# Kernel optimization log

Hardware: AMD Instinct MI355X
Metric: run time of the kernel (lower is better)

The kernel has to match this reference:

```python
import jax, jax.numpy as jnp
import numpy as np

B, S, W = 64, 128, 16
VOCAB, CVOCAB = 50000, 100
WDIM, CDIM, NF = 300, 50, 50
KS = [3, 4, 5]
HID, NLAYERS, NLAB = 256, 2, 5
COMB = WDIM + NF * len(KS)  # 450


def glorot(key, shape):
    fan_in, fan_out = shape[-2], shape[-1]
    lim = jnp.sqrt(6.0 / (fan_in + fan_out))
    return jax.random.uniform(key, shape, minval=-lim, maxval=lim, dtype=jnp.float32)


def setup_inputs() -> dict:
    key = jax.random.key(0)
    ks = jax.random.split(key, 32)
    word_ids = jax.random.randint(ks[0], (B, S), 1, VOCAB)
    char_ids = jax.random.randint(ks[1], (B, S, W), 1, CVOCAB)
    labels = jax.random.randint(ks[2], (B, S), 0, NLAB)
    lengths = jax.random.randint(ks[3], (B,), S // 2, S + 1)
    # embeddings
    word_emb = jax.random.normal(ks[4], (VOCAB, WDIM), jnp.float32) * 0.1
    word_emb = word_emb.at[0].set(0.0)
    char_emb = jax.random.normal(ks[5], (CVOCAB, CDIM), jnp.float32) * 0.1
    char_emb = char_emb.at[0].set(0.0)
    # char conv kernels: [ks, CDIM, NF] each, plus bias
    conv_w = [glorot(ks[6 + i], (k, CDIM, NF)) for i, k in enumerate(KS)]
    conv_b = [jnp.zeros((NF,), jnp.float32) for _ in KS]
    # LSTM params per layer per direction: W_ih [in,4H], W_hh [H,4H], b [4H]
    lstm = []
    kidx = 10
    in_dim = COMB
    for layer in range(NLAYERS):
        for d in range(2):
            Wih = glorot(ks[kidx], (in_dim, 4 * HID)); kidx += 1
            Whh = glorot(ks[kidx], (HID, 4 * HID)); kidx += 1
            b = jnp.zeros((4 * HID,), jnp.float32)
            lstm.extend([Wih, Whh, b])
        in_dim = 2 * HID
    out_w = glorot(ks[kidx], (2 * HID, NLAB)); kidx += 1
    out_b = jnp.zeros((NLAB,), jnp.float32)
    crf_start = jax.random.normal(ks[kidx], (NLAB,), jnp.float32) * 0.1; kidx += 1
    crf_end = jax.random.normal(ks[kidx], (NLAB,), jnp.float32) * 0.1; kidx += 1
    crf_trans = jax.random.normal(ks[kidx], (NLAB, NLAB), jnp.float32) * 0.1
    d = {
        'word_ids': word_ids, 'char_ids': char_ids, 'labels': labels, 'lengths': lengths,
        'word_emb': word_emb, 'char_emb': char_emb,
        'conv_w3': conv_w[0], 'conv_b3': conv_b[0],
        'conv_w4': conv_w[1], 'conv_b4': conv_b[1],
        'conv_w5': conv_w[2], 'conv_b5': conv_b[2],
        'out_w': out_w, 'out_b': out_b,
        'crf_start': crf_start, 'crf_end': crf_end, 'crf_trans': crf_trans,
    }
    names = ['Wih', 'Whh', 'b']
    i = 0
    for layer in range(NLAYERS):
        for dname in ['f', 'r']:
            for n in names:
                d[f'lstm_{n}_l{layer}{dname}'] = lstm[i]; i += 1
    return d


def _conv1d_same(x, w, b, pad):
    # x: [N, L, Cin], w: [k, Cin, Cout] -> [N, L_out, Cout]
    out = jax.lax.conv_general_dilated(x, w, window_strides=(1,), padding=[(pad, pad)],
                                       dimension_numbers=('NWC', 'WIO', 'NWC'))
    return out + b


def _lstm_dir(x, Wih, Whh, b, reverse):
    # x: [B, S, in] -> [B, S, H]; gate order i,f,g,o (torch convention)
    xg = jnp.einsum('bsi,ij->bsj', x, Wih) + b  # [B,S,4H]
    if reverse:
        xg = xg[:, ::-1]
    def step(carry, g):
        h, c = carry
        g = g + h @ Whh
        i, f, gg, o = jnp.split(g, 4, axis=-1)
        i, f, o = jax.nn.sigmoid(i), jax.nn.sigmoid(f), jax.nn.sigmoid(o)
        c = f * c + i * jnp.tanh(gg)
        h = o * jnp.tanh(c)
        return (h, c), h
    h0 = jnp.zeros((x.shape[0], HID), x.dtype)
    _, hs = jax.lax.scan(step, (h0, h0), jnp.swapaxes(xg, 0, 1))
    hs = jnp.swapaxes(hs, 0, 1)
    if reverse:
        hs = hs[:, ::-1]
    return hs


def reference(word_ids, char_ids, labels, lengths, word_emb, char_emb,
              conv_w3, conv_b3, conv_w4, conv_b4, conv_w5, conv_b5,
              out_w, out_b, crf_start, crf_end, crf_trans,
              lstm_Wih_l0f, lstm_Whh_l0f, lstm_b_l0f,
              lstm_Wih_l0r, lstm_Whh_l0r, lstm_b_l0r,
              lstm_Wih_l1f, lstm_Whh_l1f, lstm_b_l1f,
              lstm_Wih_l1r, lstm_Whh_l1r, lstm_b_l1r):
    # char CNN
    ce = char_emb[char_ids.reshape(-1, W)]  # [B*S, W, CDIM]
    pooled = []
    for w, b, k in [(conv_w3, conv_b3, 3), (conv_w4, conv_b4, 4), (conv_w5, conv_b5, 5)]:
        o = jax.nn.relu(_conv1d_same(ce, w, b, k // 2))
        pooled.append(jnp.max(o, axis=1))  # [B*S, NF]
    char_repr = jnp.concatenate(pooled, axis=-1).reshape(B, S, NF * len(KS))
    we = word_emb[word_ids]
    x = jnp.concatenate([we, char_repr], axis=-1)  # [B,S,COMB]
    # BiLSTM 2 layers (dropout disabled / eval mode)
    h_f = _lstm_dir(x, lstm_Wih_l0f, lstm_Whh_l0f, lstm_b_l0f, False)
    h_r = _lstm_dir(x, lstm_Wih_l0r, lstm_Whh_l0r, lstm_b_l0r, True)
    x = jnp.concatenate([h_f, h_r], axis=-1)
    h_f = _lstm_dir(x, lstm_Wih_l1f, lstm_Whh_l1f, lstm_b_l1f, False)
    h_r = _lstm_dir(x, lstm_Wih_l1r, lstm_Whh_l1r, lstm_b_l1r, True)
    x = jnp.concatenate([h_f, h_r], axis=-1)
    emissions = jnp.einsum('bsh,hl->bsl', x, out_w) + out_b  # [B,S,NLAB]
    # CRF NLL (pytorch-crf, batch_first, reduction='mean')
    mask = (jnp.arange(S)[None, :] < lengths[:, None])  # [B,S] bool
    maskf = mask.astype(emissions.dtype)
    tags = labels  # already in [0,NLAB)
    # numerator: score of gold path
    em_score = jnp.take_along_axis(emissions, tags[..., None], axis=-1)[..., 0]  # [B,S]
    num = crf_start[tags[:, 0]] + em_score[:, 0]
    trans_score = crf_trans[tags[:, :-1], tags[:, 1:]]  # [B,S-1]
    num = num + jnp.sum((trans_score + em_score[:, 1:]) * maskf[:, 1:], axis=1)
    last_idx = lengths - 1
    last_tag = jnp.take_along_axis(tags, last_idx[:, None], axis=1)[:, 0]
    num = num + crf_end[last_tag]
    # denominator: forward algorithm via scan
    alpha0 = crf_start + emissions[:, 0]  # [B,NLAB]
    def step(alpha, inp):
        em_t, m_t = inp  # [B,NLAB], [B]
        nxt = jax.nn.logsumexp(alpha[:, :, None] + crf_trans[None], axis=1) + em_t
        alpha = jnp.where(m_t[:, None], nxt, alpha)
        return alpha, None
    alpha, _ = jax.lax.scan(step, alpha0,
                            (jnp.swapaxes(emissions[:, 1:], 0, 1), jnp.swapaxes(mask[:, 1:], 0, 1)))
    denom = jax.nn.logsumexp(alpha + crf_end[None], axis=1)  # [B]
    llh = num - denom
    return -jnp.mean(llh)
```

## Files before the change

### kernel.cpp

```cpp
#include <hip/hip_runtime.h>
#include <hip/hip_fp16.h>
#include <math.h>
#include <stdint.h>

#define NB   64
#define NS   128
#define NW   16
#define CD   50
#define NF_  50
#define WD   300
#define COMB 450
#define K2P0 240
#define K2P1 256
#define HID  256
#define G4   1024
#define NLAB 5

#define WHH_SW4  (7.0f / 0.06846532f)
#define WHH_INV4 (1.0f / (WHH_SW4 * 7.0f))

#define CW_S   (7.0f / 0.24494897f)
#define EMB_S  14.0f
#define CONV_INV (1.0f / (CW_S * EMB_S))

typedef _Float16 h2_t __attribute__((ext_vector_type(2)));
typedef _Float16 v8h  __attribute__((ext_vector_type(8)));
typedef float    v16f __attribute__((ext_vector_type(16)));

__device__ __forceinline__ float sigf(float x)   { return 1.0f / (1.0f + __expf(-x)); }
__device__ __forceinline__ float tanhf_(float x) { return 1.0f - 2.0f / (__expf(2.0f * x) + 1.0f); }

__device__ __forceinline__ int sdot8f(uint32_t a, int b, int acc) {
#if __has_builtin(__builtin_amdgcn_sdot8)
    return __builtin_amdgcn_sdot8((int)a, b, acc, false);
#else
#pragma unroll
    for (int i = 0; i < 8; ++i) {
        int av = ((int)(a << (28 - 4 * i))) >> 28;
        int bv = ((int)(((uint32_t)b) << (28 - 4 * i))) >> 28;
        acc += av * bv;
    }
    return acc;
#endif
}

__device__ __forceinline__ uint32_t packh2(float lo, float hi) {
    __half l = __float2half(lo), h = __float2half(hi);
    return ((uint32_t)__half_as_ushort(h) << 16) | (uint32_t)__half_as_ushort(l);
}

__device__ __forceinline__ int q4clamp(float v, float s) {
    int q = (int)rintf(v * s);
    return q < -7 ? -7 : (q > 7 ? 7 : q);
}

#define PK_CONV_END 17
#define PK_WIH0_END (17 + 1920)
#define PK_WIH1_END (PK_WIH0_END + 2048)
#define PK_END      (PK_WIH1_END + 512)

__global__ __launch_bounds__(256) void pack_all(
    const float* __restrict__ w3, const float* __restrict__ w4,
    const float* __restrict__ w5, uint32_t* __restrict__ cwq,
    const float* __restrict__ Wih0f, const float* __restrict__ Wih0r,
    const float* __restrict__ Wih1f, const float* __restrict__ Wih1r,
    uint32_t* __restrict__ P0f, uint32_t* __restrict__ P0r,
    uint32_t* __restrict__ P1f, uint32_t* __restrict__ P1r,
    const float* __restrict__ Whh0f, const float* __restrict__ Whh0r,
    const float* __restrict__ Whh1f, const float* __restrict__ Whh1r,
    uint32_t* __restrict__ Q0f, uint32_t* __restrict__ Q0r,
    uint32_t* __restrict__ Q1f, uint32_t* __restrict__ Q1r)
{
    int blk = blockIdx.x;
    int tid = threadIdx.x;

    if (blk < PK_CONV_END) {
        int idx = blk * 256 + tid;
        if (idx >= 4200) return;
        const float* W; int rel;
        if (idx < 1050)       { W = w3; rel = idx; }
        else if (idx < 2450)  { W = w4; rel = idx - 1050; }
        else                  { W = w5; rel = idx - 2450; }
        int t = rel / 350, r2 = rel - t * 350;
        int wi = r2 / 50, f = r2 - wi * 50;
        uint32_t out = 0;
#pragma unroll
        for (int j = 0; j < 8; ++j) {
            int c = wi * 8 + j;
            if (c < CD) {
                int q = q4clamp(W[(size_t)(t * CD + c) * NF_ + f], CW_S);
                out |= ((uint32_t)(q & 0xF)) << (4 * j);
            }
        }
        cwq[idx] = out;
    } else if (blk < PK_WIH1_END) {
        int layer, dir, rel;
        if (blk < PK_WIH0_END) { layer = 0; rel = blk - PK_CONV_END; dir = rel / 960;  rel %= 960; }
        else                   { layer = 1; rel = blk - PK_WIH0_END; dir = rel / 1024; rel %= 1024; }
        int K   = layer ? 512 : COMB;
        int K2P = layer ? K2P1 : K2P0;
        const float* W = layer ? (dir ? Wih1r : Wih1f) : (dir ? Wih0r : Wih0f);
        uint32_t* P    = layer ? (dir ? P1r : P1f) : (dir ? P0r : P0f);
        int idx = rel * 256 + tid;
        if (idx >= K2P * 1024) return;
        int n = idx & 1023, kp = idx >> 10;
        uint32_t v = 0;
        if (2 * kp + 1 < K) {
            __half l = __float2half(W[(size_t)(2 * kp) * 1024 + n]);
            __half h = __float2half(W[(size_t)(2 * kp + 1) * 1024 + n]);
            v = ((uint32_t)__half_as_ushort(h) << 16) | (uint32_t)__half_as_ushort(l);
        }
        P[((size_t)(kp >> 2) * 1024 + n) * 4 + (kp & 3)] = v;
    } else {
        int rel = blk - PK_WIH1_END;
        int which = rel >> 7;
        const float* W; uint32_t* Q;
        switch (which) {
            case 0:  W = Whh0f; Q = Q0f; break;
            case 1:  W = Whh0r; Q = Q0r; break;
            case 2:  W = Whh1f; Q = Q1f; break;
            default: W = Whh1r; Q = Q1r; break;
        }
        int idx = (rel & 127) * 256 + tid;
        int m = idx & 3, col = (idx >> 2) & 1023, iq = idx >> 12;
        int kbase = (iq * 4 + m) * 8;
        uint32_t out = 0;
#pragma unroll
        for (int j = 0; j < 8; ++j) {
            int q = q4clamp(W[(size_t)(kbase + j) * G4 + col], WHH_SW4);
            out |= ((uint32_t)(q & 0xF)) << (4 * j);
        }
        Q[idx] = out;
    }
}

__global__ __launch_bounds__(512) void cnn_embed4(
    const int* __restrict__ word_ids, const int* __restrict__ char_ids,
    const float* __restrict__ word_emb, const float* __restrict__ char_emb,
    const uint32_t* __restrict__ cwq,
    const float* __restrict__ b3, const float* __restrict__ b4,
    const float* __restrict__ b5, uint32_t* __restrict__ x0p)
{
    __shared__ uint32_t cws[4200];
    __shared__ uint32_t cepq[8][NW][7];
    int tid  = threadIdx.x;
    int g    = tid >> 6;
    int lane = tid & 63;
    int pos  = blockIdx.x * 8 + g;

    for (int i = tid; i < 4200; i += 512) cws[i] = cwq[i];

    const int* cid = char_ids + (size_t)pos * NW;
    for (int idx = lane; idx < NW * 7; idx += 64) {
        int w  = idx / 7;
        int wi = idx - w * 7;
        const float* e = char_emb + (size_t)cid[w] * CD + 8 * wi;
        int nc = CD - 8 * wi; if (nc > 8) nc = 8;
        uint32_t pk = 0;
        for (int j = 0; j < nc; ++j) {
            float v = e[j];
            v = v > 0.5f ? 0.5f : (v < -0.5f ? -0.5f : v);
            int q = q4clamp(v, EMB_S);
            pk |= ((uint32_t)(q & 0xF)) << (4 * j);
        }
        cepq[g][w][wi] = pk;
    }
    {
        int wid = word_ids[pos];
        const float* src = word_emb + (size_t)wid * WD;
        uint32_t* dst = x0p + (size_t)pos * K2P0;
        for (int idx = lane; idx < 150; idx += 64) {
            float2 v = *(const float2*)(src + 2 * idx);
            dst[idx] = packh2(v.x, v.y);
        }
        for (int idx = lane; idx < 15; idx += 64) dst[225 + idx] = 0;
    }
    __syncthreads();

    int f = lane;
    float m3 = 0.f, m4 = 0.f, m5 = 0.f;
    if (f < NF_) {
        int a3[16] = {}, a4[17] = {}, a5[16] = {};
        for (int wi = 0; wi < 7; ++wi) {
            uint32_t w3q[3], w4q[4], w5q[5];
#pragma unroll
            for (int t = 0; t < 3; ++t) w3q[t] = cws[(t * 7 + wi) * NF_ + f];
#pragma unroll
            for (int t = 0; t < 4; ++t) w4q[t] = cws[1050 + (t * 7 + wi) * NF_ + f];
#pragma unroll
            for (int t = 0; t < 5; ++t) w5q[t] = cws[2450 + (t * 7 + wi) * NF_ + f];
#pragma unroll
            for (int ip = 0; ip < 16; ++ip) {
                uint32_t e = cepq[g][ip][wi];
#pragma unroll
                for (int t = 0; t < 3; ++t) { int p = ip + 1 - t; if (p >= 0 && p < 16) a3[p] = sdot8f(e, (int)w3q[t], a3[p]); }
#pragma unroll
                for (int t = 0; t < 4; ++t) { int p = ip + 2 - t; if (p >= 0 && p < 17) a4[p] = sdot8f(e, (int)w4q[t], a4[p]); }
#pragma unroll
                for (int t = 0; t < 5; ++t) { int p = ip + 2 - t; if (p >= 0 && p < 16) a5[p] = sdot8f(e, (int)w5q[t], a5[p]); }
            }
        }
        int i3 = a3[0], i4 = a4[0], i5 = a5[0];
#pragma unroll
        for (int p = 1; p < 16; ++p) { i3 = max(i3, a3[p]); i5 = max(i5, a5[p]); }
#pragma unroll
        for (int p = 1; p < 17; ++p) i4 = max(i4, a4[p]);
        m3 = fmaxf(0.f, (float)i3 * CONV_INV + b3[f]);
        m4 = fmaxf(0.f, (float)i4 * CONV_INV + b4[f]);
        m5 = fmaxf(0.f, (float)i5 * CONV_INV + b5[f]);
    }
    float m3x = __shfl_xor(m3, 1);
    float m4x = __shfl_xor(m4, 1);
    float m5x = __shfl_xor(m5, 1);
    if (f < NF_ && !(f & 1)) {
        int i = f >> 1;
        uint32_t* dst = x0p + (size_t)pos * K2P0 + 150;
        dst[i]      = packh2(m3, m3x);
        dst[25 + i] = packh2(m4, m4x);
        dst[50 + i] = packh2(m5, m5x);
    }
}

__global__ __launch_bounds__(256) void gemm_mfma(
    const uint32_t* __restrict__ Ap, int K2,
    const uint32_t* __restrict__ Wpf, const uint32_t* __restrict__ Wpr,
    const float* __restrict__ bf, const float* __restrict__ br,
    float* __restrict__ Cf, float* __restrict__ Cr)
{
    int by  = blockIdx.y;
    int dir = by >> 4;
    int n0  = (by & 15) * 64;
    int m0  = blockIdx.x * 128;
    const uint32_t* Wp = dir ? Wpr : Wpf;
    const float* bias  = dir ? br : bf;
    float* C           = dir ? Cr : Cf;

    int tid = threadIdx.x;
    int w = tid >> 6, l = tid & 63;
    int l31 = l & 31, lk = l >> 5;

    const uint32_t* arow = Ap + (size_t)(m0 + w * 32 + l31) * K2 + lk * 4;
    const uint4*    bq0  = (const uint4*)(Wp) + (size_t)lk * 1024 + n0 + l31;

    v16f acc0 = {}, acc1 = {};

    for (int kp0 = 0; kp0 < K2; kp0 += 8) {
        uint4 av = *(const uint4*)(arow + kp0);
        const uint4* bq = bq0 + (size_t)(kp0 >> 2) * 1024;
        uint4 b0v = bq[0];
        uint4 b1v = bq[32];
        v8h af = __builtin_bit_cast(v8h, av);
        acc0 = __builtin_amdgcn_mfma_f32_32x32x16_f16(af, __builtin_bit_cast(v8h, b0v), acc0, 0, 0, 0);
        acc1 = __builtin_amdgcn_mfma_f32_32x32x16_f16(af, __builtin_bit_cast(v8h, b1v), acc1, 0, 0, 0);
    }

#pragma unroll
    for (int r = 0; r < 16; ++r) {
        int row = m0 + w * 32 + (r & 3) + 8 * (r >> 2) + 4 * lk;
        int c0 = n0 + l31, c1 = n0 + 32 + l31;
        C[(size_t)row * G4 + c0] = acc0[r] + bias[c0];
        C[(size_t)row * G4 + c1] = acc1[r] + bias[c1];
    }
}

__global__ __launch_bounds__(512, 1) void lstm_rec14(
    const float* __restrict__ xg_f, const float* __restrict__ xg_r,
    const uint32_t* __restrict__ Qf, const uint32_t* __restrict__ Qr,
    uint32_t* __restrict__ outp)
{
    int bid = blockIdx.x;
    int b = bid >> 1, d = bid & 1;
    const float* xg = d ? xg_r : xg_f;
    const uint4* Q4 = (const uint4*)(d ? Qr : Qf);

    __shared__ uint32_t hp8[32];
    __shared__ float gates[G4];
    __shared__ alignas(16) uint4 Tl[4 * 1024];

    int t = threadIdx.x;
    int lane = t & 63;

    uint4 rA[4], rB[4];
#pragma unroll
    for (int iq = 0; iq < 4; ++iq) {
        rA[iq] = Q4[(size_t)iq * 1024 + t];
        rB[iq] = Q4[(size_t)iq * 1024 + t + 512];
    }
    for (int i = t; i < 4 * 1024; i += 512) Tl[i] = Q4[4 * 1024 + i];
    if (t < 32) hp8[t] = 0;
    float cst = 0.f;

    int te0 = d ? (NS - 1) : 0;
    size_t prow = ((size_t)b * NS + te0) * G4;
    float xA = xg[prow + t];
    float xB = xg[prow + 512 + t];
    __syncthreads();

    for (int s = 0; s < NS; ++s) {
        int te = d ? (NS - 1 - s) : s;
        int row = b * NS + te;

        float nxA = 0.f, nxB = 0.f;
        if (s + 1 < NS) {
            int te1 = d ? (NS - 2 - s) : (s + 1);
            size_t r1 = ((size_t)b * NS + te1) * G4;
            nxA = xg[r1 + t];
            nxB = xg[r1 + 512 + t];
        }

        int hreg = (int)hp8[lane & 31];
        int a0 = 0, a1 = 0;

#pragma unroll
        for (int iq = 0; iq < 4; ++iq) {
            int h0 = __builtin_amdgcn_readlane(hreg, 4 * iq);
            int h1 = __builtin_amdgcn_readlane(hreg, 4 * iq + 1);
            int h2 = __builtin_amdgcn_readlane(hreg, 4 * iq + 2);
            int h3 = __builtin_amdgcn_readlane(hreg, 4 * iq + 3);
            a0 = sdot8f(rA[iq].x, h0, a0); a0 = sdot8f(rA[iq].y, h1, a0);
            a0 = sdot8f(rA[iq].z, h2, a0); a0 = sdot8f(rA[iq].w, h3, a0);
            a1 = sdot8f(rB[iq].x, h0, a1); a1 = sdot8f(rB[iq].y, h1, a1);
            a1 = sdot8f(rB[iq].z, h2, a1); a1 = sdot8f(rB[iq].w, h3, a1);
        }
#pragma unroll
        for (int iq2 = 0; iq2 < 4; ++iq2) {
            uint4 wa = Tl[iq2 * 1024 + t];
            uint4 wb = Tl[iq2 * 1024 + t + 512];
            int h0 = __builtin_amdgcn_readlane(hreg, 16 + 4 * iq2);
            int h1 = __builtin_amdgcn_readlane(hreg, 17 + 4 * iq2);
            int h2 = __builtin_amdgcn_readlane(hreg, 18 + 4 * iq2);
            int h3 = __builtin_amdgcn_readlane(hreg, 19 + 4 * iq2);
            a0 = sdot8f(wa.x, h0, a0); a0 = sdot8f(wa.y, h1, a0);
            a0 = sdot8f(wa.z, h2, a0); a0 = sdot8f(wa.w, h3, a0);
            a1 = sdot8f(wb.x, h0, a1); a1 = sdot8f(wb.y, h1, a1);
            a1 = sdot8f(wb.z, h2, a1); a1 = sdot8f(wb.w, h3, a1);
        }

        gates[t]       = (float)a0 * WHH_INV4 + xA;
        gates[t + 512] = (float)a1 * WHH_INV4 + xB;
        __syncthreads();
        if (t < 256) {
            int j = t;
            float gi = gates[j];
            float gf = gates[256 + j];
            float gg = gates[512 + j];
            float go = gates[768 + j];
            float ii = sigf(gi), ff = sigf(gf), g2 = tanhf_(gg), oo = sigf(go);
            cst = ff * cst + ii * g2;
            float h = oo * tanhf_(cst);
            int q = (int)rintf(h * 7.0f);
            q = q < -7 ? -7 : (q > 7 ? 7 : q);
            int qx = __shfl_xor(q, 1);
            float hx = __shfl_xor(h, 1);
            if (!(t & 1)) {
                ((unsigned char*)hp8)[j >> 1] =
                    (unsigned char)((q & 0xF) | ((qx & 0xF) << 4));
                outp[(size_t)row * 256 + d * 128 + (j >> 1)] = packh2(h, hx);
            }
        }
        xA = nxA; xB = nxB;
        __syncthreads();
    }
}

__global__ __launch_bounds__(256) void emis_kernel(
    const uint32_t* __restrict__ x2p, const float* __restrict__ ow,
    const float* __restrict__ ob, float* __restrict__ em)
{
    int i = blockIdx.x * blockDim.x + threadIdx.x;
    if (i >= NB * NS) return;
    const uint32_t* xr = x2p + (size_t)i * 256;
    float acc[NLAB];
#pragma unroll
    for (int l = 0; l < NLAB; ++l) acc[l] = ob[l];
    for (int p = 0; p < 256; ++p) {
        h2_t hv = __builtin_bit_cast(h2_t, xr[p]);
        float lo = (float)hv[0], hi = (float)hv[1];
        int k = 2 * p;
#pragma unroll
        for (int l = 0; l < NLAB; ++l)
            acc[l] += lo * ow[(size_t)k * NLAB + l] + hi * ow[(size_t)(k + 1) * NLAB + l];
    }
    float* e = em + (size_t)i * NLAB;
#pragma unroll
    for (int l = 0; l < NLAB; ++l) e[l] = acc[l];
}

__device__ __forceinline__ float lse5(const float* v) {
    float m = fmaxf(fmaxf(fmaxf(v[0], v[1]), fmaxf(v[2], v[3])), v[4]);
    float s = __expf(v[0] - m) + __expf(v[1] - m) + __expf(v[2] - m) +
              __expf(v[3] - m) + __expf(v[4] - m);
    return m + __logf(s);
}

__global__ __launch_bounds__(64) void crf_kernel(
    const float* __restrict__ em, const int* __restrict__ labels,
    const int* __restrict__ lengths, const float* __restrict__ cstart,
    const float* __restrict__ cend, const float* __restrict__ ctrans,
    float* __restrict__ outp)
{
    __shared__ float tr_s[25], st_s[5], en_s[5];
    int tid = threadIdx.x;
    if (tid < 25) tr_s[tid] = ctrans[tid];
    if (tid < 5)  { st_s[tid] = cstart[tid]; en_s[tid] = cend[tid]; }
    __syncthreads();

    int b = tid;
    int len = lengths[b];
    const int* tg = labels + (size_t)b * NS;
    const float* eb = em + (size_t)b * NS * NLAB;

    int prev = tg[0];
    float num = st_s[prev] + eb[prev];
    for (int t = 1; t < NS; ++t) {
        if (t < len) {
            int cur = tg[t];
            num += tr_s[prev * NLAB + cur] + eb[t * NLAB + cur];
            prev = cur;
        }
    }
    num += en_s[tg[len - 1]];

    float a[NLAB];
#pragma unroll
    for (int y = 0; y < NLAB; ++y) a[y] = st_s[y] + eb[y];
    for (int t = 1; t < NS; ++t) {
        if (t < len) {
            float na[NLAB];
#pragma unroll
            for (int y = 0; y < NLAB; ++y) {
                float v[NLAB];
#pragma unroll
                for (int x = 0; x < NLAB; ++x) v[x] = a[x] + tr_s[x * NLAB + y];
                na[y] = lse5(v) + eb[t * NLAB + y];
            }
#pragma unroll
            for (int y = 0; y < NLAB; ++y) a[y] = na[y];
        }
    }
    float v[NLAB];
#pragma unroll
    for (int y = 0; y < NLAB; ++y) v[y] = a[y] + en_s[y];
    float denom = lse5(v);

    float llh = num - denom;
#pragma unroll
    for (int off = 32; off > 0; off >>= 1) llh += __shfl_down(llh, off);
    if (tid == 0) outp[0] = -llh * (1.0f / 64.0f);
}

extern "C" void kernel_launch(void* const* d_in, const int* in_sizes, int n_in,
                              void* d_out, int out_size, void* d_ws, size_t ws_size,
                              hipStream_t stream)
{
    const int*   word_ids = (const int*)d_in[0];
    const int*   char_ids = (const int*)d_in[1];
    const int*   labels   = (const int*)d_in[2];
    const int*   lengths  = (const int*)d_in[3];
    const float* word_emb = (const float*)d_in[4];
    const float* char_emb = (const float*)d_in[5];
    const float* cw3 = (const float*)d_in[6];
    const float* cb3 = (const float*)d_in[7];
    const float* cw4 = (const float*)d_in[8];
    const float* cb4 = (const float*)d_in[9];
    const float* cw5 = (const float*)d_in[10];
    const float* cb5 = (const float*)d_in[11];
    const float* out_w = (const float*)d_in[12];
    const float* out_b = (const float*)d_in[13];
    const float* crf_start = (const float*)d_in[14];
    const float* crf_end   = (const float*)d_in[15];
    const float* crf_trans = (const float*)d_in[16];
    const float* Wih_l0f = (const float*)d_in[17];
    const float* Whh_l0f = (const float*)d_in[18];
    const float* b_l0f   = (const float*)d_in[19];
    const float* Wih_l0r = (const float*)d_in[20];
    const float* Whh_l0r = (const float*)d_in[21];
    const float* b_l0r   = (const float*)d_in[22];
    const float* Wih_l1f = (const float*)d_in[23];
    const float* Whh_l1f = (const float*)d_in[24];
    const float* b_l1f   = (const float*)d_in[25];
    const float* Wih_l1r = (const float*)d_in[26];
    const float* Whh_l1r = (const float*)d_in[27];
    const float* b_l1r   = (const float*)d_in[28];

    uint32_t* wsu = (uint32_t*)d_ws;
    uint32_t* x0p  = wsu;
    float*    xg_f = (float*)(wsu + 1966080);
    float*    xg_r = xg_f + 8388608;
    uint32_t* x1p  = (uint32_t*)(xg_r + 8388608);
    uint32_t* x2p  = x1p + 2097152;
    float*    em   = (float*)(x2p + 2097152);
    uint32_t* wp0f = (uint32_t*)(em + 40960);
    uint32_t* wp0r = wp0f + 245760;
    uint32_t* wp1f = wp0r + 245760;
    uint32_t* wp1r = wp1f + 262144;
    uint32_t* cwq  = wp1r + 262144;
    uint32_t* wh0f = cwq  + 4200;
    uint32_t* wh0r = wh0f + 32768;
    uint32_t* wh1f = wh0r + 32768;
    uint32_t* wh1r = wh1f + 32768;

    pack_all<<<PK_END, 256, 0, stream>>>(
        cw3, cw4, cw5, cwq,
        Wih_l0f, Wih_l0r, Wih_l1f, Wih_l1r, wp0f, wp0r, wp1f, wp1r,
        Whh_l0f, Whh_l0r, Whh_l1f, Whh_l1r, wh0f, wh0r, wh1f, wh1r);

    cnn_embed4<<<1024, 512, 0, stream>>>(word_ids, char_ids, word_emb, char_emb,
                                         cwq, cb3, cb4, cb5, x0p);

    dim3 gGemm(64, 32);
    gemm_mfma<<<gGemm, 256, 0, stream>>>(x0p, K2P0, wp0f, wp0r, b_l0f, b_l0r, xg_f, xg_r);

    lstm_rec14<<<128, 512, 0, stream>>>(xg_f, xg_r, wh0f, wh0r, x1p);

    gemm_mfma<<<gGemm, 256, 0, stream>>>(x1p, K2P1, wp1f, wp1r, b_l1f, b_l1r, xg_f, xg_r);

    lstm_rec14<<<128, 512, 0, stream>>>(xg_f, xg_r, wh1f, wh1r, x2p);

    emis_kernel<<<32, 256, 0, stream>>>(x2p, out_w, out_b, em);
    crf_kernel<<<1, 64, 0, stream>>>(em, labels, lengths, crf_start, crf_end, crf_trans,
                                     (float*)d_out);
}
```

Before: 492.9 us.

## Keep all recurrent weights in registers and parallelize emission projection per row

```diff
diff --git a/kernel.cpp b/kernel.cpp
--- a/kernel.cpp
+++ b/kernel.cpp
@@ -263,7 +263,7 @@
     }
 }
 
-__global__ __launch_bounds__(512, 1) void lstm_rec14(
+__global__ __launch_bounds__(512, 1) void lstm_rec17(
     const float* __restrict__ xg_f, const float* __restrict__ xg_r,
     const uint32_t* __restrict__ Qf, const uint32_t* __restrict__ Qr,
     uint32_t* __restrict__ outp)
@@ -275,18 +275,16 @@
 
     __shared__ uint32_t hp8[32];
     __shared__ float gates[G4];
-    __shared__ alignas(16) uint4 Tl[4 * 1024];
 
     int t = threadIdx.x;
     int lane = t & 63;
 
-    uint4 rA[4], rB[4];
-#pragma unroll
-    for (int iq = 0; iq < 4; ++iq) {
+    uint4 rA[8], rB[8];
+#pragma unroll
+    for (int iq = 0; iq < 8; ++iq) {
         rA[iq] = Q4[(size_t)iq * 1024 + t];
         rB[iq] = Q4[(size_t)iq * 1024 + t + 512];
     }
-    for (int i = t; i < 4 * 1024; i += 512) Tl[i] = Q4[4 * 1024 + i];
     if (t < 32) hp8[t] = 0;
     float cst = 0.f;
 
@@ -309,35 +307,22 @@
         }
 
         int hreg = (int)hp8[lane & 31];
-        int a0 = 0, a1 = 0;
-
-#pragma unroll
-        for (int iq = 0; iq < 4; ++iq) {
+        int a0 = 0, a0b = 0, a1 = 0, a1b = 0;
+
+#pragma unroll
+        for (int iq = 0; iq < 8; ++iq) {
             int h0 = __builtin_amdgcn_readlane(hreg, 4 * iq);
             int h1 = __builtin_amdgcn_readlane(hreg, 4 * iq + 1);
             int h2 = __builtin_amdgcn_readlane(hreg, 4 * iq + 2);
             int h3 = __builtin_amdgcn_readlane(hreg, 4 * iq + 3);
-            a0 = sdot8f(rA[iq].x, h0, a0); a0 = sdot8f(rA[iq].y, h1, a0);
-            a0 = sdot8f(rA[iq].z, h2, a0); a0 = sdot8f(rA[iq].w, h3, a0);
-            a1 = sdot8f(rB[iq].x, h0, a1); a1 = sdot8f(rB[iq].y, h1, a1);
-            a1 = sdot8f(rB[iq].z, h2, a1); a1 = sdot8f(rB[iq].w, h3, a1);
-        }
-#pragma unroll
-        for (int iq2 = 0; iq2 < 4; ++iq2) {
-            uint4 wa = Tl[iq2 * 1024 + t];
-            uint4 wb = Tl[iq2 * 1024 + t + 512];
-            int h0 = __builtin_amdgcn_readlane(hreg, 16 + 4 * iq2);
-            int h1 = __builtin_amdgcn_readlane(hreg, 17 + 4 * iq2);
-            int h2 = __builtin_amdgcn_readlane(hreg, 18 + 4 * iq2);
-            int h3 = __builtin_amdgcn_readlane(hreg, 19 + 4 * iq2);
-            a0 = sdot8f(wa.x, h0, a0); a0 = sdot8f(wa.y, h1, a0);
-            a0 = sdot8f(wa.z, h2, a0); a0 = sdot8f(wa.w, h3, a0);
-            a1 = sdot8f(wb.x, h0, a1); a1 = sdot8f(wb.y, h1, a1);
-            a1 = sdot8f(wb.z, h2, a1); a1 = sdot8f(wb.w, h3, a1);
-        }
-
-        gates[t]       = (float)a0 * WHH_INV4 + xA;
-        gates[t + 512] = (float)a1 * WHH_INV4 + xB;
+            a0  = sdot8f(rA[iq].x, h0, a0);  a0b = sdot8f(rA[iq].y, h1, a0b);
+            a0  = sdot8f(rA[iq].z, h2, a0);  a0b = sdot8f(rA[iq].w, h3, a0b);
+            a1  = sdot8f(rB[iq].x, h0, a1);  a1b = sdot8f(rB[iq].y, h1, a1b);
+            a1  = sdot8f(rB[iq].z, h2, a1);  a1b = sdot8f(rB[iq].w, h3, a1b);
+        }
+
+        gates[t]       = (float)(a0 + a0b) * WHH_INV4 + xA;
+        gates[t + 512] = (float)(a1 + a1b) * WHH_INV4 + xB;
         __syncthreads();
         if (t < 256) {
             int j = t;
@@ -363,27 +348,42 @@
     }
 }
 
-__global__ __launch_bounds__(256) void emis_kernel(
+__global__ __launch_bounds__(256) void emis_kernel2(
     const uint32_t* __restrict__ x2p, const float* __restrict__ ow,
     const float* __restrict__ ob, float* __restrict__ em)
 {
-    int i = blockIdx.x * blockDim.x + threadIdx.x;
-    if (i >= NB * NS) return;
-    const uint32_t* xr = x2p + (size_t)i * 256;
-    float acc[NLAB];
-#pragma unroll
-    for (int l = 0; l < NLAB; ++l) acc[l] = ob[l];
-    for (int p = 0; p < 256; ++p) {
+    __shared__ float ows[2560];
+    __shared__ float obs[NLAB];
+    int tid = threadIdx.x;
+    for (int i = tid; i < 2560; i += 256) ows[i] = ow[i];
+    if (tid < NLAB) obs[tid] = ob[tid];
+    __syncthreads();
+
+    int wv = tid >> 6, lane = tid & 63;
+    int row = blockIdx.x * 4 + wv;
+    const uint32_t* xr = x2p + (size_t)row * 256;
+
+    float acc[NLAB] = {};
+#pragma unroll
+    for (int m = 0; m < 4; ++m) {
+        int p = lane + 64 * m;
         h2_t hv = __builtin_bit_cast(h2_t, xr[p]);
         float lo = (float)hv[0], hi = (float)hv[1];
         int k = 2 * p;
 #pragma unroll
         for (int l = 0; l < NLAB; ++l)
-            acc[l] += lo * ow[(size_t)k * NLAB + l] + hi * ow[(size_t)(k + 1) * NLAB + l];
-    }
-    float* e = em + (size_t)i * NLAB;
-#pragma unroll
-    for (int l = 0; l < NLAB; ++l) e[l] = acc[l];
+            acc[l] += lo * ows[k * NLAB + l] + hi * ows[(k + 1) * NLAB + l];
+    }
+#pragma unroll
+    for (int off = 32; off > 0; off >>= 1)
+#pragma unroll
+        for (int l = 0; l < NLAB; ++l) acc[l] += __shfl_down(acc[l], off);
+    if (lane < NLAB) {  }
+    if (lane == 0) {
+#pragma unroll
+        for (int l = 0; l < NLAB; ++l)
+            em[(size_t)row * NLAB + l] = acc[l] + obs[l];
+    }
 }
 
 __device__ __forceinline__ float lse5(const float* v) {
@@ -511,13 +511,13 @@
     dim3 gGemm(64, 32);
     gemm_mfma<<<gGemm, 256, 0, stream>>>(x0p, K2P0, wp0f, wp0r, b_l0f, b_l0r, xg_f, xg_r);
 
-    lstm_rec14<<<128, 512, 0, stream>>>(xg_f, xg_r, wh0f, wh0r, x1p);
+    lstm_rec17<<<128, 512, 0, stream>>>(xg_f, xg_r, wh0f, wh0r, x1p);
 
     gemm_mfma<<<gGemm, 256, 0, stream>>>(x1p, K2P1, wp1f, wp1r, b_l1f, b_l1r, xg_f, xg_r);
 
-    lstm_rec14<<<128, 512, 0, stream>>>(xg_f, xg_r, wh1f, wh1r, x2p);
-
-    emis_kernel<<<32, 256, 0, stream>>>(x2p, out_w, out_b, em);
+    lstm_rec17<<<128, 512, 0, stream>>>(xg_f, xg_r, wh1f, wh1r, x2p);
+
+    emis_kernel2<<<2048, 256, 0, stream>>>(x2p, out_w, out_b, em);
     crf_kernel<<<1, 64, 0, stream>>>(em, labels, lengths, crf_start, crf_end, crf_trans,
                                      (float*)d_out);
 }
```

Measured after the change: 454.5 us. -7.8%, faster.
